# Kernel optimization log

Measured on AMD Instinct MI355X. Metric: run time of the kernel, lower is better.

## Reference

```python
import jax, jax.numpy as jnp
import numpy as np

DIM = 1024
GROUPS = 32
EPS = 1e-5


def setup_inputs() -> dict:
    key = jax.random.key(0)
    ks = jax.random.split(key, 12)
    b, c, h, w = 16, DIM, 32, 32  # h*w must equal DIM for GroupNorm(32, dim) on (b, hw, c)
    x = jax.random.normal(ks[0], (b, c, h, w), dtype=jnp.float32)
    # GroupNorm affine params: num_channels = dim (applied along hw axis, which == dim)
    gamma = jnp.ones((DIM,), dtype=jnp.float32)
    beta = jnp.zeros((DIM,), dtype=jnp.float32)
    init = lambda k: jax.random.normal(k, (DIM, DIM), dtype=jnp.float32) * 0.02
    Wq, Wk, Wv, Wo = init(ks[1]), init(ks[2]), init(ks[3]), init(ks[4])
    bq = jax.random.normal(ks[5], (DIM,), dtype=jnp.float32) * 0.02
    bk = jax.random.normal(ks[6], (DIM,), dtype=jnp.float32) * 0.02
    bv = jax.random.normal(ks[7], (DIM,), dtype=jnp.float32) * 0.02
    bo = jax.random.normal(ks[8], (DIM,), dtype=jnp.float32) * 0.02
    return {"x": x, "gamma": gamma, "beta": beta,
            "Wq": Wq, "bq": bq, "Wk": Wk, "bk": bk,
            "Wv": Wv, "bv": bv, "Wo": Wo, "bo": bo}


def _group_norm(x, gamma, beta):
    # x: (b, N, c) where N == num_channels (torch GroupNorm normalizes groups along dim 1)
    b, N, c = x.shape
    xg = x.reshape(b, GROUPS, (N // GROUPS) * c)
    mean = xg.mean(-1, keepdims=True)
    var = xg.var(-1, keepdims=True)
    xn = ((xg - mean) * jax.lax.rsqrt(var + EPS)).reshape(b, N, c)
    return xn * gamma[None, :, None] + beta[None, :, None]


def reference(x, gamma, beta, Wq, bq, Wk, bk, Wv, bv, Wo, bo):
    b, c, h, w = x.shape
    xs = x.reshape(b, c, h * w).transpose(0, 2, 1)  # (b, N, c), N = h*w
    norm_x = _group_norm(xs, gamma, beta)
    q = norm_x @ Wq.T + bq
    k = norm_x @ Wk.T + bk
    v = norm_x @ Wv.T + bv
    attn = jnp.einsum('bqd,bkd->bqk', q, k) * (c ** -0.5)
    attn = jax.nn.softmax(attn, axis=-1)
    # Faithful to original: 'bqk,bvd->bqd' sums k and v independently (no contraction between them)
    out = jnp.einsum('bqk,bvd->bqd', attn, v)
    out = out @ Wo.T + bo  # Dropout(p=0.0) is identity
    return out.transpose(0, 2, 1).reshape(b, c, h, w)
```

## Files before the change

kernel.cpp:

```cpp
#include <hip/hip_runtime.h>


#define BATCH 16
#define CH    1024
#define NHW   1024
#define G     32
#define NPG   32
#define EPG   (NPG*CH)
#define EPSV  1e-5f

__global__ __launch_bounds__(256) void k1_stats_pw(
    const float* __restrict__ x, const float* __restrict__ gamma,
    float* __restrict__ pw, float2* __restrict__ s1s2)
{
    const int bg = blockIdx.x;
    const int b  = bg >> 5, g = bg & 31;
    const int t  = threadIdx.x;
    const int n4 = t & 7;
    const int c0 = t >> 3;

    const float4* xg = reinterpret_cast<const float4*>(x + (size_t)b * (CH * NHW) + g * NPG);
    const float4  gm = reinterpret_cast<const float4*>(gamma + g * NPG)[n4];

    float s1 = 0.f, s2 = 0.f;
    float* pwrow = pw + (size_t)bg * CH;
    for (int ch = c0; ch < CH; ch += 32) {
        float4 v = xg[ch * (NHW / 4) + n4];
        s1 += v.x + v.y + v.z + v.w;
        s2 += v.x * v.x + v.y * v.y + v.z * v.z + v.w * v.w;
        float p = v.x * gm.x + v.y * gm.y + v.z * gm.z + v.w * gm.w;
        p += __shfl_xor(p, 1);
        p += __shfl_xor(p, 2);
        p += __shfl_xor(p, 4);
        if (n4 == 0) pwrow[ch] = p;
    }
    #pragma unroll
    for (int m = 1; m < 64; m <<= 1) { s1 += __shfl_xor(s1, m); s2 += __shfl_xor(s2, m); }
    __shared__ float r1[4], r2[4];
    if ((t & 63) == 0) { r1[t >> 6] = s1; r2[t >> 6] = s2; }
    __syncthreads();
    if (t == 0) s1s2[bg] = make_float2(r1[0] + r1[1] + r1[2] + r1[3],
                                       r2[0] + r2[1] + r2[2] + r2[3]);
}

__global__ __launch_bounds__(256) void k2_colsum(
    const float* __restrict__ pw, const float2* __restrict__ s1s2,
    const float* __restrict__ gamma, const float* __restrict__ beta,
    float* __restrict__ colsum)
{
    const int b = blockIdx.x;
    const int t = threadIdx.x;
    __shared__ float invg[G], meang[G], sgg[G];
    __shared__ float wred[4];
    __shared__ float constb;

    if (t < G) {
        float2 s   = s1s2[b * G + t];
        float mean = s.x * (1.f / EPG);
        float var  = s.y * (1.f / EPG) - mean * mean;
        invg[t]  = rsqrtf(var + EPSV);
        meang[t] = mean;
        float sg = 0.f;
        for (int i = 0; i < NPG; i++) sg += gamma[t * NPG + i];
        sgg[t] = sg;
    }
    float bsum = beta[t] + beta[t + 256] + beta[t + 512] + beta[t + 768];
    #pragma unroll
    for (int m = 1; m < 64; m <<= 1) bsum += __shfl_xor(bsum, m);
    if ((t & 63) == 0) wred[t >> 6] = bsum;
    __syncthreads();
    if (t == 0) {
        float cb = wred[0] + wred[1] + wred[2] + wred[3];
        for (int g = 0; g < G; g++) cb -= invg[g] * meang[g] * sgg[g];
        constb = cb;
    }
    __syncthreads();
    for (int ch = t; ch < CH; ch += 256) {
        float cs = constb;
        const float* p = pw + (size_t)b * (G * CH) + ch;
        #pragma unroll 8
        for (int g = 0; g < G; g++) cs += invg[g] * p[g * CH];
        colsum[b * CH + ch] = cs;
    }
}

__global__ __launch_bounds__(256) void k3_matvec_v(
    const float* __restrict__ Wv, const float* __restrict__ bv,
    const float* __restrict__ colsum, float* __restrict__ S)
{
    const int t = threadIdx.x;
    const int wave = t >> 6, lane = t & 63;
    const int d = blockIdx.x * 4 + wave;
    const float* wrow = Wv + (size_t)d * CH;
    float acc[BATCH];
    #pragma unroll
    for (int b = 0; b < BATCH; b++) acc[b] = 0.f;
    for (int e = lane; e < CH; e += 64) {
        float w = wrow[e];
        #pragma unroll
        for (int b = 0; b < BATCH; b++) acc[b] += w * colsum[b * CH + e];
    }
    #pragma unroll
    for (int b = 0; b < BATCH; b++) {
        float a = acc[b];
        #pragma unroll
        for (int m = 1; m < 64; m <<= 1) a += __shfl_xor(a, m);
        if (lane == 0) S[b * CH + d] = a + (float)NHW * bv[d];
    }
}

__global__ __launch_bounds__(256) void k4_final_bcast(
    const float* __restrict__ Wo, const float* __restrict__ bo,
    const float* __restrict__ S, float* __restrict__ out)
{
    const int t = threadIdx.x;
    const int wave = t >> 6, lane = t & 63;
    const int d = blockIdx.x * 4 + wave;
    const float* wrow = Wo + (size_t)d * CH;
    float acc[BATCH];
    #pragma unroll
    for (int b = 0; b < BATCH; b++) acc[b] = 0.f;
    for (int e = lane; e < CH; e += 64) {
        float w = wrow[e];
        #pragma unroll
        for (int b = 0; b < BATCH; b++) acc[b] += w * S[b * CH + e];
    }
    #pragma unroll
    for (int b = 0; b < BATCH; b++) {
        #pragma unroll
        for (int m = 1; m < 64; m <<= 1) acc[b] += __shfl_xor(acc[b], m);
    }
    const float bod = bo[d];
    #pragma unroll
    for (int b = 0; b < BATCH; b++) {
        float val = acc[b] + bod;
        float4 v4 = make_float4(val, val, val, val);
        float4* op = reinterpret_cast<float4*>(out + ((size_t)b * CH + d) * NHW);
        #pragma unroll
        for (int i = 0; i < 4; i++) op[i * 64 + lane] = v4;
    }
}

extern "C" void kernel_launch(void* const* d_in, const int* in_sizes, int n_in,
                              void* d_out, int out_size, void* d_ws, size_t ws_size,
                              hipStream_t stream)
{
    const float* x     = (const float*)d_in[0];
    const float* gamma = (const float*)d_in[1];
    const float* beta  = (const float*)d_in[2];
    const float* Wv    = (const float*)d_in[7];
    const float* bv    = (const float*)d_in[8];
    const float* Wo    = (const float*)d_in[9];
    const float* bo    = (const float*)d_in[10];
    float* out = (float*)d_out;

    char* ws = (char*)d_ws;
    float*  pw     = (float*)ws;
    float2* s1s2   = (float2*)(ws + (size_t)524288 * 4);
    float*  colsum = (float*)(ws + (size_t)524288 * 4 + 4096);
    float*  Sbuf   = (float*)(ws + (size_t)524288 * 4 + 4096 + 65536);

    k1_stats_pw   <<<BATCH * G, 256, 0, stream>>>(x, gamma, pw, s1s2);
    k2_colsum     <<<BATCH,     256, 0, stream>>>(pw, s1s2, gamma, beta, colsum);
    k3_matvec_v   <<<NHW / 4,   256, 0, stream>>>(Wv, bv, colsum, Sbuf);
    k4_final_bcast<<<NHW / 4,   256, 0, stream>>>(Wo, bo, Sbuf, out);
}
```

Baseline: 186.1 us.

## Fuse group stats and column-sum into one kernel via atomics; vectorize matvecs

```diff
diff --git a/kernel.cpp b/kernel.cpp
--- a/kernel.cpp
+++ b/kernel.cpp
@@ -9,21 +9,24 @@
 #define EPG   (NPG*CH)
 #define EPSV  1e-5f
 
-__global__ __launch_bounds__(256) void k1_stats_pw(
+__global__ __launch_bounds__(256) void k1_fused(
     const float* __restrict__ x, const float* __restrict__ gamma,
-    float* __restrict__ pw, float2* __restrict__ s1s2)
+    const float* __restrict__ beta, float* __restrict__ colsum)
 {
     const int bg = blockIdx.x;
     const int b  = bg >> 5, g = bg & 31;
     const int t  = threadIdx.x;
+    const int lane = t & 63, wave = t >> 6;
     const int n4 = t & 7;
     const int c0 = t >> 3;
+
+    __shared__ float pch[CH];
+    __shared__ float r1[4], r2[4], rb[4];
 
     const float4* xg = reinterpret_cast<const float4*>(x + (size_t)b * (CH * NHW) + g * NPG);
     const float4  gm = reinterpret_cast<const float4*>(gamma + g * NPG)[n4];
 
     float s1 = 0.f, s2 = 0.f;
-    float* pwrow = pw + (size_t)bg * CH;
     for (int ch = c0; ch < CH; ch += 32) {
         float4 v = xg[ch * (NHW / 4) + n4];
         s1 += v.x + v.y + v.z + v.w;
@@ -32,56 +35,30 @@
         p += __shfl_xor(p, 1);
         p += __shfl_xor(p, 2);
         p += __shfl_xor(p, 4);
-        if (n4 == 0) pwrow[ch] = p;
-    }
-    #pragma unroll
-    for (int m = 1; m < 64; m <<= 1) { s1 += __shfl_xor(s1, m); s2 += __shfl_xor(s2, m); }
-    __shared__ float r1[4], r2[4];
-    if ((t & 63) == 0) { r1[t >> 6] = s1; r2[t >> 6] = s2; }
-    __syncthreads();
-    if (t == 0) s1s2[bg] = make_float2(r1[0] + r1[1] + r1[2] + r1[3],
-                                       r2[0] + r2[1] + r2[2] + r2[3]);
-}
-
-__global__ __launch_bounds__(256) void k2_colsum(
-    const float* __restrict__ pw, const float2* __restrict__ s1s2,
-    const float* __restrict__ gamma, const float* __restrict__ beta,
-    float* __restrict__ colsum)
-{
-    const int b = blockIdx.x;
-    const int t = threadIdx.x;
-    __shared__ float invg[G], meang[G], sgg[G];
-    __shared__ float wred[4];
-    __shared__ float constb;
-
-    if (t < G) {
-        float2 s   = s1s2[b * G + t];
-        float mean = s.x * (1.f / EPG);
-        float var  = s.y * (1.f / EPG) - mean * mean;
-        invg[t]  = rsqrtf(var + EPSV);
-        meang[t] = mean;
-        float sg = 0.f;
-        for (int i = 0; i < NPG; i++) sg += gamma[t * NPG + i];
-        sgg[t] = sg;
+        if (n4 == 0) pch[ch] = p;
     }
     float bsum = beta[t] + beta[t + 256] + beta[t + 512] + beta[t + 768];
     #pragma unroll
-    for (int m = 1; m < 64; m <<= 1) bsum += __shfl_xor(bsum, m);
-    if ((t & 63) == 0) wred[t >> 6] = bsum;
+    for (int m = 1; m < 64; m <<= 1) {
+        s1 += __shfl_xor(s1, m); s2 += __shfl_xor(s2, m); bsum += __shfl_xor(bsum, m);
+    }
+    if (lane == 0) { r1[wave] = s1; r2[wave] = s2; rb[wave] = bsum; }
     __syncthreads();
-    if (t == 0) {
-        float cb = wred[0] + wred[1] + wred[2] + wred[3];
-        for (int g = 0; g < G; g++) cb -= invg[g] * meang[g] * sgg[g];
-        constb = cb;
-    }
-    __syncthreads();
-    for (int ch = t; ch < CH; ch += 256) {
-        float cs = constb;
-        const float* p = pw + (size_t)b * (G * CH) + ch;
-        #pragma unroll 8
-        for (int g = 0; g < G; g++) cs += invg[g] * p[g * CH];
-        colsum[b * CH + ch] = cs;
-    }
+
+    const float S1 = r1[0] + r1[1] + r1[2] + r1[3];
+    const float S2 = r2[0] + r2[1] + r2[2] + r2[3];
+    const float SB = rb[0] + rb[1] + rb[2] + rb[3];
+    const float mean = S1 * (1.f / EPG);
+    const float var  = S2 * (1.f / EPG) - mean * mean;
+    const float inv  = rsqrtf(var + EPSV);
+    float sg = gm.x + gm.y + gm.z + gm.w;
+    sg += __shfl_xor(sg, 1);
+    sg += __shfl_xor(sg, 2);
+    sg += __shfl_xor(sg, 4);
+    const float cshare = SB * (1.f / 32.f) - inv * mean * sg;
+
+    for (int ch = t; ch < CH; ch += 256)
+        atomicAdd(&colsum[b * CH + ch], inv * pch[ch] + cshare);
 }
 
 __global__ __launch_bounds__(256) void k3_matvec_v(
@@ -91,14 +68,20 @@
     const int t = threadIdx.x;
     const int wave = t >> 6, lane = t & 63;
     const int d = blockIdx.x * 4 + wave;
-    const float* wrow = Wv + (size_t)d * CH;
+    const float4* wrow = reinterpret_cast<const float4*>(Wv + (size_t)d * CH);
+    const float4* cs4  = reinterpret_cast<const float4*>(colsum);
     float acc[BATCH];
     #pragma unroll
     for (int b = 0; b < BATCH; b++) acc[b] = 0.f;
-    for (int e = lane; e < CH; e += 64) {
-        float w = wrow[e];
+    #pragma unroll
+    for (int i = 0; i < 4; i++) {
+        int e4 = i * 64 + lane;
+        float4 w = wrow[e4];
         #pragma unroll
-        for (int b = 0; b < BATCH; b++) acc[b] += w * colsum[b * CH + e];
+        for (int b = 0; b < BATCH; b++) {
+            float4 c = cs4[b * 256 + e4];
+            acc[b] += w.x * c.x + w.y * c.y + w.z * c.z + w.w * c.w;
+        }
     }
     #pragma unroll
     for (int b = 0; b < BATCH; b++) {
@@ -116,14 +99,20 @@
     const int t = threadIdx.x;
     const int wave = t >> 6, lane = t & 63;
     const int d = blockIdx.x * 4 + wave;
-    const float* wrow = Wo + (size_t)d * CH;
+    const float4* wrow = reinterpret_cast<const float4*>(Wo + (size_t)d * CH);
+    const float4* s4   = reinterpret_cast<const float4*>(S);
     float acc[BATCH];
     #pragma unroll
     for (int b = 0; b < BATCH; b++) acc[b] = 0.f;
-    for (int e = lane; e < CH; e += 64) {
-        float w = wrow[e];
+    #pragma unroll
+    for (int i = 0; i < 4; i++) {
+        int e4 = i * 64 + lane;
+        float4 w = wrow[e4];
         #pragma unroll
-        for (int b = 0; b < BATCH; b++) acc[b] += w * S[b * CH + e];
+        for (int b = 0; b < BATCH; b++) {
+            float4 c = s4[b * 256 + e4];
+            acc[b] += w.x * c.x + w.y * c.y + w.z * c.z + w.w * c.w;
+        }
     }
     #pragma unroll
     for (int b = 0; b < BATCH; b++) {
@@ -155,13 +144,11 @@
     float* out = (float*)d_out;
 
     char* ws = (char*)d_ws;
-    float*  pw     = (float*)ws;
-    float2* s1s2   = (float2*)(ws + (size_t)524288 * 4);
-    float*  colsum = (float*)(ws + (size_t)524288 * 4 + 4096);
-    float*  Sbuf   = (float*)(ws + (size_t)524288 * 4 + 4096 + 65536);
+    float* colsum = (float*)ws;
+    float* Sbuf   = (float*)(ws + 65536);
 
-    k1_stats_pw   <<<BATCH * G, 256, 0, stream>>>(x, gamma, pw, s1s2);
-    k2_colsum     <<<BATCH,     256, 0, stream>>>(pw, s1s2, gamma, beta, colsum);
+    hipMemsetAsync(colsum, 0, BATCH * CH * sizeof(float), stream);
+    k1_fused      <<<BATCH * G, 256, 0, stream>>>(x, gamma, beta, colsum);
     k3_matvec_v   <<<NHW / 4,   256, 0, stream>>>(Wv, bv, colsum, Sbuf);
     k4_final_bcast<<<NHW / 4,   256, 0, stream>>>(Wo, bo, Sbuf, out);
 }
```

New measurement: 179.0 us. 1.04x faster.
